# Kernel optimization log

Hardware: AMD Instinct MI355X
Metric: run time of the kernel (lower is better)

Reference implementation:

```python
import jax, jax.numpy as jnp
import numpy as np

N, E = 10000, 320000
D_IN, H1, REP, PRED_HID = 512, 512, 256, 512
TOPK = 4
EPS = 1e-5


def l2norm(x):
    return x / jnp.sqrt(jnp.sum(x * x, axis=-1, keepdims=True) + 1e-12)


def gcn_conv(x, row, col, W, b):
    # PyG GCNConv: add self loops, symmetric normalization, aggregate at col
    n = x.shape[0]
    ar = jnp.arange(n)
    r = jnp.concatenate([row, ar])
    c = jnp.concatenate([col, ar])
    w = jnp.ones(r.shape[0], x.dtype)
    deg = jax.ops.segment_sum(w, c, num_segments=n)
    dis = jnp.where(deg > 0, jax.lax.rsqrt(jnp.maximum(deg, 1e-12)), 0.0)
    norm = dis[r] * dis[c]  # [E+N]
    h = x @ W               # [N, out]
    out = jax.ops.segment_sum(norm[:, None] * h[r], c, num_segments=n)
    return out + b


def batchnorm(x, g, b):
    m = jnp.mean(x, axis=0)
    v = jnp.var(x, axis=0)
    return (x - m) * jax.lax.rsqrt(v + EPS) * g + b


def prelu(x, a):
    return jnp.where(x > 0, x, a * x)


def encoder(x, row, col, params):
    for (W, b, g, bt, a) in params:
        x = prelu(batchnorm(gcn_conv(x, row, col, W, b), g, bt), a)
    return x


def predictor(x, pW1, pb1, pg, pbb, pa, pW2, pb2):
    h = x @ pW1 + pb1
    h = prelu(batchnorm(h, pg, pbb), pa)
    return h @ pW2 + pb2


def setup_inputs():
    key = jax.random.key(0)
    ks = jax.random.split(key, 8)
    def rnd(k, shape, s=0.05):
        return jax.random.normal(k, shape, jnp.float32) * s
    return dict(
        x=jax.random.normal(ks[0], (N, D_IN), jnp.float32),
        edge_index=jax.random.randint(ks[1], (2, E), 0, N),
        neighbor_index=jax.random.randint(ks[2], (2, E), 0, N),
        W1=rnd(ks[3], (D_IN, H1)), b1=jnp.zeros((H1,), jnp.float32),
        bn1_g=jnp.ones((H1,), jnp.float32), bn1_b=jnp.zeros((H1,), jnp.float32),
        pr1=jnp.full((1,), 0.25, jnp.float32),
        W2=rnd(ks[4], (H1, REP)), b2=jnp.zeros((REP,), jnp.float32),
        bn2_g=jnp.ones((REP,), jnp.float32), bn2_b=jnp.zeros((REP,), jnp.float32),
        pr2=jnp.full((1,), 0.25, jnp.float32),
        pW1=rnd(ks[5], (REP, PRED_HID)), pb1=jnp.zeros((PRED_HID,), jnp.float32),
        pbn_g=jnp.ones((PRED_HID,), jnp.float32), pbn_b=jnp.zeros((PRED_HID,), jnp.float32),
        ppr=jnp.full((1,), 0.25, jnp.float32),
        pW2=rnd(ks[6], (PRED_HID, REP)), pb2=jnp.zeros((REP,), jnp.float32),
    )


def reference(x, edge_index, neighbor_index, W1, b1, bn1_g, bn1_b, pr1,
              W2, b2, bn2_g, bn2_b, pr2,
              pW1, pb1, pbn_g, pbn_b, ppr, pW2, pb2):
    n = x.shape[0]
    row, col = edge_index[0], edge_index[1]
    params = [(W1, b1, bn1_g, bn1_b, pr1), (W2, b2, bn2_g, bn2_b, pr2)]
    student = encoder(x, row, col, params)
    # teacher = deepcopy of student encoder at init (same params), no grad
    teacher = jax.lax.stop_gradient(encoder(x, row, col, params))
    pred = predictor(student, pW1, pb1, pbn_g, pbn_b, ppr, pW2, pb2)

    # augment_adj: per-edge similarity of normalized embeddings, densify, topk
    sn, tn = l2norm(student), l2norm(teacher)
    nrow, ncol = neighbor_index[0], neighbor_index[1]
    sim_e = jnp.sum(sn[nrow] * tn[ncol], axis=-1)                 # [E]
    S = jnp.zeros((n, n), jnp.float32).at[nrow, ncol].add(sim_e)  # coalesce sums dups
    A = jnp.zeros((n, n), jnp.bool_).at[nrow, ncol].set(True)
    _, I_knn = jax.lax.top_k(S, TOPK - 1)                          # [N, TOPK-1]

    # id loss over positive-pair levels (BGRL/AFGRL-style cosine loss)
    pn, tgt = l2norm(pred), l2norm(teacher)
    ar = jnp.arange(n)
    terms = [jnp.mean(2.0 - 2.0 * jnp.sum(pn * tgt, axis=-1))]     # self pairs
    for i in range(TOPK - 1):
        nb = I_knn[:, i]
        mask = A[ar, nb].astype(jnp.float32)  # locality = knn * adj
        c = jnp.sum(pn * tgt[nb], axis=-1)
        terms.append(jnp.sum(mask * (2.0 - 2.0 * c)) / jnp.maximum(jnp.sum(mask), 1.0))
    loss = sum(terms) / len(terms)
    return student, loss
```

## Files before the change

kernel.cpp:

```cpp
#include <hip/hip_runtime.h>
#include <math.h>

#define NN 10000
#define NE 320000
#define NXE (NE / 8)
#define SPAD 20
#define BSTR (8 * SPAD)
#define PAD 96

typedef __attribute__((ext_vector_type(8))) short bf16x8;
typedef __attribute__((ext_vector_type(4))) float f32x4;

__device__ inline unsigned short f2bf(float f) {
  unsigned u = __float_as_uint(f);
  unsigned r = (u + 0x7fffu + ((u >> 16) & 1u)) >> 16;
  return (unsigned short)r;
}
__device__ inline float bflo(unsigned u) { return __uint_as_float(u << 16); }
__device__ inline float bfhi(unsigned u) { return __uint_as_float(u & 0xffff0000u); }

#define X4 (NN * 512 / 4)
#define W1N (512 * 512)
#define W2N (512 * 256)
#define P1N (256 * 512)
#define P2N (512 * 256)
#define S1 X4
#define S2 (S1 + W1N)
#define S3 (S2 + W2N)
#define S4 (S3 + P1N)
#define PREP_TOT (S4 + P2N)

__global__ void prep_kernel(const float* __restrict__ x, unsigned short* __restrict__ xb,
    const float* __restrict__ W1, unsigned short* __restrict__ W1t,
    const float* __restrict__ W2, unsigned short* __restrict__ W2t,
    const float* __restrict__ pW1, unsigned short* __restrict__ pW1t,
    const float* __restrict__ pW2, unsigned short* __restrict__ pW2t) {
  for (int i = blockIdx.x * blockDim.x + threadIdx.x; i < PREP_TOT;
       i += gridDim.x * blockDim.x) {
    if (i < X4) {
      const float4 v = reinterpret_cast<const float4*>(x)[i];
      ushort4 o;
      o.x = f2bf(v.x); o.y = f2bf(v.y); o.z = f2bf(v.z); o.w = f2bf(v.w);
      reinterpret_cast<ushort4*>(xb)[i] = o;
    } else if (i < S2) {
      const int j = i - S1, n = j >> 9, k = j & 511;
      W1t[j] = f2bf(W1[(size_t)k * 512 + n]);
    } else if (i < S3) {
      const int j = i - S2, n = j >> 9, k = j & 511;
      W2t[j] = f2bf(W2[(size_t)k * 256 + n]);
    } else if (i < S4) {
      const int j = i - S3, n = j >> 8, k = j & 255;
      pW1t[j] = f2bf(pW1[(size_t)k * 512 + n]);
    } else {
      const int j = i - S4, n = j >> 9, k = j & 511;
      pW2t[j] = f2bf(pW2[(size_t)k * 256 + n]);
    }
  }
}

#define GBM 128
#define GBN 64
#define GBK 32
#define SAS 40

template <bool BF16OUT>
__global__ __launch_bounds__(256) void gemm_bf16(
    const unsigned short* __restrict__ A, const unsigned short* __restrict__ Bt,
    const float* __restrict__ bias, const float* __restrict__ rowscale,
    float* __restrict__ Cf, unsigned short* __restrict__ Cb,
    int M, int N, int K) {
  __shared__ unsigned short As[GBM * SAS];
  __shared__ unsigned short Bs[GBN * SAS];
  const int bm = blockIdx.y * GBM;
  const int bn = blockIdx.x * GBN;
  const int tid = threadIdx.x;
  const int wave = tid >> 6, lane = tid & 63;
  const int wm = wave & 1, wn = wave >> 1;
  f32x4 acc[4][2] = {};

  const int srow = tid >> 2;
  const int scol = (tid & 3) << 3;

  for (int k0 = 0; k0 < K; k0 += GBK) {
#pragma unroll
    for (int r = 0; r < 2; ++r) {
      const int row = srow + (r << 6);
      const int gr = bm + row;
      uint4 v = make_uint4(0u, 0u, 0u, 0u);
      if (gr < M) v = *reinterpret_cast<const uint4*>(&A[(size_t)gr * K + k0 + scol]);
      *reinterpret_cast<uint4*>(&As[row * SAS + scol]) = v;
    }
    {
      const uint4 v = *reinterpret_cast<const uint4*>(
          &Bt[(size_t)(bn + srow) * K + k0 + scol]);
      *reinterpret_cast<uint4*>(&Bs[srow * SAS + scol]) = v;
    }
    __syncthreads();
    const int kofs = (lane >> 4) << 3;
    const int rl = lane & 15;
    bf16x8 af[4], bfr[2];
#pragma unroll
    for (int m = 0; m < 4; ++m)
      af[m] = *reinterpret_cast<const bf16x8*>(
          &As[((wm << 6) + (m << 4) + rl) * SAS + kofs]);
#pragma unroll
    for (int n = 0; n < 2; ++n)
      bfr[n] = *reinterpret_cast<const bf16x8*>(
          &Bs[((wn << 5) + (n << 4) + rl) * SAS + kofs]);
#pragma unroll
    for (int m = 0; m < 4; ++m)
#pragma unroll
      for (int n = 0; n < 2; ++n)
        acc[m][n] = __builtin_amdgcn_mfma_f32_16x16x32_bf16(af[m], bfr[n], acc[m][n], 0, 0, 0);
    __syncthreads();
  }
  const int crow0 = (lane >> 4) << 2;
  const int ccol = lane & 15;
#pragma unroll
  for (int n = 0; n < 2; ++n) {
    const int col = bn + (wn << 5) + (n << 4) + ccol;
    const float bv = (!BF16OUT && bias) ? bias[col] : 0.f;
#pragma unroll
    for (int m = 0; m < 4; ++m) {
#pragma unroll
      for (int r = 0; r < 4; ++r) {
        const int rowg = bm + (wm << 6) + (m << 4) + crow0 + r;
        if (rowg < M) {
          if (BF16OUT)
            Cb[(size_t)rowg * N + col] = f2bf(acc[m][n][r] * rowscale[rowg]);
          else
            Cf[(size_t)rowg * N + col] = acc[m][n][r] + bv;
        }
      }
    }
  }
}

__global__ __launch_bounds__(256) void fill_pad8(
    const int* __restrict__ col, const int* __restrict__ row,
    int* __restrict__ cur1, unsigned short* __restrict__ ridx,
    const int* __restrict__ nrow, const int* __restrict__ ncol,
    int* __restrict__ cur2, unsigned short* __restrict__ ncidx) {
  const int x = blockIdx.x & 7;
  const int p = blockIdx.x >> 3;
  const int o = p * 256 + threadIdx.x;
  if (o >= NXE) return;
  const int e = x * NXE + o;
  {
    const int k = col[e];
    const int s = atomicAdd(&cur1[x * NN + k], 1);
    if (s < SPAD) ridx[(size_t)k * BSTR + x * SPAD + s] = (unsigned short)row[e];
  }
  {
    const int k = nrow[e];
    const int s = atomicAdd(&cur2[x * NN + k], 1);
    if (s < SPAD) ncidx[(size_t)k * BSTR + x * SPAD + s] = (unsigned short)ncol[e];
  }
}

__global__ __launch_bounds__(128) void compact_dis(
    const int* __restrict__ cur1, const unsigned short* __restrict__ rin,
    int* __restrict__ deg1, float* __restrict__ dis, unsigned short* __restrict__ rout,
    const int* __restrict__ cur2, const unsigned short* __restrict__ nin,
    int* __restrict__ deg2, unsigned short* __restrict__ nout) {
  const int j = blockIdx.x * 2 + (threadIdx.x >> 6);
  const int lane = threadIdx.x & 63;
  {
    int pre[9]; pre[0] = 0; int raw = 0;
#pragma unroll
    for (int x = 0; x < 8; ++x) {
      const int c = cur1[x * NN + j];
      raw += c;
      pre[x + 1] = pre[x] + min(c, SPAD);
    }
    const int degc = min(pre[8], PAD);
    if (lane == 0) {
      deg1[j] = degc;
      dis[j] = 1.0f / sqrtf((float)(raw + 1));
    }
    for (int t = lane; t < degc; t += 64) {
      int x = 0;
      while (t >= pre[x + 1]) ++x;
      rout[(size_t)j * PAD + t] = rin[(size_t)j * BSTR + x * SPAD + (t - pre[x])];
    }
  }
  {
    int pre[9]; pre[0] = 0;
#pragma unroll
    for (int x = 0; x < 8; ++x)
      pre[x + 1] = pre[x] + min(cur2[x * NN + j], SPAD);
    const int degc = min(pre[8], PAD);
    if (lane == 0) deg2[j] = degc;
    for (int t = lane; t < degc; t += 64) {
      int x = 0;
      while (t >= pre[x + 1]) ++x;
      nout[(size_t)j * PAD + t] = nin[(size_t)j * BSTR + x * SPAD + (t - pre[x])];
    }
  }
}

template <int C>
__global__ __launch_bounds__(128) void gcn_slice(const unsigned short* __restrict__ hs,
    const float* __restrict__ dis, const int* __restrict__ deg,
    const unsigned short* __restrict__ ridx, const float* __restrict__ bias,
    float* __restrict__ out) {
  constexpr int NS = C / 128;
  const int b = blockIdx.x;
  const int x = b & 7;
  const int p = b >> 3;
  const int slice = x & (NS - 1);
  const int pair = p * (8 / NS) + (x / NS);
  const int wave = threadIdx.x >> 6;
  const int lane = threadIdx.x & 63;
  const int j = pair * 2 + wave;
  const int g = lane >> 4;
  const int l = lane & 15;
  const int cbase = slice * 128 + l * 8;
  const unsigned short* hb = hs + cbase;

  float a[8];
  if (g == 0) {
    const uint4 v = *reinterpret_cast<const uint4*>(hb + (size_t)j * C);
    a[0] = bflo(v.x); a[1] = bfhi(v.x); a[2] = bflo(v.y); a[3] = bfhi(v.y);
    a[4] = bflo(v.z); a[5] = bfhi(v.z); a[6] = bflo(v.w); a[7] = bfhi(v.w);
  } else {
#pragma unroll
    for (int c = 0; c < 8; ++c) a[c] = 0.f;
  }
  const int e0 = j * PAD;
  const int e1 = e0 + min(deg[j], PAD);
  int e = e0 + g;
  for (; e + 4 < e1; e += 8) {
    const int r0 = ridx[e], r1 = ridx[e + 4];
    const uint4 v0 = *reinterpret_cast<const uint4*>(hb + (size_t)r0 * C);
    const uint4 v1 = *reinterpret_cast<const uint4*>(hb + (size_t)r1 * C);
    a[0] += bflo(v0.x) + bflo(v1.x); a[1] += bfhi(v0.x) + bfhi(v1.x);
    a[2] += bflo(v0.y) + bflo(v1.y); a[3] += bfhi(v0.y) + bfhi(v1.y);
    a[4] += bflo(v0.z) + bflo(v1.z); a[5] += bfhi(v0.z) + bfhi(v1.z);
    a[6] += bflo(v0.w) + bflo(v1.w); a[7] += bfhi(v0.w) + bfhi(v1.w);
  }
  if (e < e1) {
    const uint4 v = *reinterpret_cast<const uint4*>(hb + (size_t)ridx[e] * C);
    a[0] += bflo(v.x); a[1] += bfhi(v.x); a[2] += bflo(v.y); a[3] += bfhi(v.y);
    a[4] += bflo(v.z); a[5] += bfhi(v.z); a[6] += bflo(v.w); a[7] += bfhi(v.w);
  }
#pragma unroll
  for (int c = 0; c < 8; ++c) {
    a[c] += __shfl_xor(a[c], 16);
    a[c] += __shfl_xor(a[c], 32);
  }
  if (g == 0) {
    const float dj = dis[j];
    const float* bs = bias + cbase;
    float4 w0, w1;
    w0.x = fmaf(dj, a[0], bs[0]); w0.y = fmaf(dj, a[1], bs[1]);
    w0.z = fmaf(dj, a[2], bs[2]); w0.w = fmaf(dj, a[3], bs[3]);
    w1.x = fmaf(dj, a[4], bs[4]); w1.y = fmaf(dj, a[5], bs[5]);
    w1.z = fmaf(dj, a[6], bs[6]); w1.w = fmaf(dj, a[7], bs[7]);
    float* o = out + (size_t)j * C + cbase;
    *reinterpret_cast<float4*>(o) = w0;
    *reinterpret_cast<float4*>(o + 4) = w1;
  }
}

template <int C>
__global__ __launch_bounds__(256) void bn_stats(const float* __restrict__ x,
    float* __restrict__ sums, float* __restrict__ sqs, int n) {
  constexpr int P = C / 256;
  float s[P], q[P];
#pragma unroll
  for (int p = 0; p < P; ++p) { s[p] = 0.f; q[p] = 0.f; }
  const int rpb = (n + gridDim.x - 1) / gridDim.x;
  const int r0 = blockIdx.x * rpb;
  const int r1 = min(r0 + rpb, n);
  for (int r = r0; r < r1; ++r) {
#pragma unroll
    for (int p = 0; p < P; ++p) {
      const float v = x[(size_t)r * C + threadIdx.x + (p << 8)];
      s[p] += v;
      q[p] = fmaf(v, v, q[p]);
    }
  }
#pragma unroll
  for (int p = 0; p < P; ++p) {
    atomicAdd(&sums[threadIdx.x + (p << 8)], s[p]);
    atomicAdd(&sqs[threadIdx.x + (p << 8)], q[p]);
  }
}

__device__ inline void bn_coeff(const float* sums, const float* sqs,
                                const float* g, const float* b, int c,
                                float inv_n, float& sc, float& sh) {
  const float m = sums[c] * inv_n;
  const float var = sqs[c] * inv_n - m * m;
  sc = g[c] / sqrtf(var + 1e-5f);
  sh = b[c] - m * sc;
}

__global__ void bn_apply_prelu(const float* __restrict__ in,
    unsigned short* __restrict__ outb, const float* __restrict__ sums,
    const float* __restrict__ sqs, const float* __restrict__ g,
    const float* __restrict__ b, const float* __restrict__ pa,
    float inv_n, int total4, int cmask) {
  const float a = pa[0];
  for (int i = blockIdx.x * blockDim.x + threadIdx.x; i < total4;
       i += gridDim.x * blockDim.x) {
    float4 v = reinterpret_cast<const float4*>(in)[i];
    const int c0 = (i << 2) & cmask;
    float r[4] = {v.x, v.y, v.z, v.w};
    ushort4 o;
    unsigned short* op = reinterpret_cast<unsigned short*>(&o);
#pragma unroll
    for (int j = 0; j < 4; ++j) {
      float sc, sh;
      bn_coeff(sums, sqs, g, b, c0 + j, inv_n, sc, sh);
      float t = fmaf(r[j], sc, sh);
      t = t > 0.f ? t : a * t;
      op[j] = f2bf(t);
    }
    reinterpret_cast<ushort4*>(outb)[i] = o;
  }
}

__global__ __launch_bounds__(128) void bn_l2_student(float* __restrict__ student,
    unsigned short* __restrict__ stb, unsigned short* __restrict__ snb,
    const float* __restrict__ sums, const float* __restrict__ sqs,
    const float* __restrict__ g, const float* __restrict__ b,
    const float* __restrict__ pa, float inv_n) {
  const int r = blockIdx.x * 2 + (threadIdx.x >> 6);
  const int t = threadIdx.x & 63;
  const float a = pa[0];
  const float4 v = reinterpret_cast<const float4*>(student + (size_t)r * 256)[t];
  float w[4] = {v.x, v.y, v.z, v.w};
  const int c0 = t << 2;
#pragma unroll
  for (int j = 0; j < 4; ++j) {
    float sc, sh;
    bn_coeff(sums, sqs, g, b, c0 + j, inv_n, sc, sh);
    float u = fmaf(w[j], sc, sh);
    w[j] = u > 0.f ? u : a * u;
  }
  reinterpret_cast<float4*>(student + (size_t)r * 256)[t] =
      make_float4(w[0], w[1], w[2], w[3]);
  ushort4 ob;
  ob.x = f2bf(w[0]); ob.y = f2bf(w[1]); ob.z = f2bf(w[2]); ob.w = f2bf(w[3]);
  reinterpret_cast<ushort4*>(stb + (size_t)r * 256)[t] = ob;
  float sq = w[0] * w[0] + w[1] * w[1] + w[2] * w[2] + w[3] * w[3];
#pragma unroll
  for (int o = 1; o < 64; o <<= 1) sq += __shfl_xor(sq, o);
  const float inv = 1.0f / sqrtf(sq + 1e-12f);
  ushort4 on;
  on.x = f2bf(w[0] * inv); on.y = f2bf(w[1] * inv);
  on.z = f2bf(w[2] * inv); on.w = f2bf(w[3] * inv);
  reinterpret_cast<ushort4*>(snb + (size_t)r * 256)[t] = on;
}

__global__ __launch_bounds__(128) void topk_kernel(const unsigned short* __restrict__ snb,
    const int* __restrict__ deg, const unsigned short* __restrict__ ncidx,
    int* __restrict__ nb) {
  const int wv = threadIdx.x >> 6, lane = threadIdx.x & 63;
  const int i = blockIdx.x * 2 + wv;
  __shared__ unsigned short sni[2][256];
  __shared__ float vals[2][PAD];
  __shared__ int   cols[2][PAD];
  __shared__ float mvals[2][PAD];
  __shared__ int   mcols[2][PAD];
  reinterpret_cast<uint2*>(sni[wv])[lane] =
      reinterpret_cast<const uint2*>(snb + (size_t)i * 256)[lane];
  __syncthreads();
  const int e0 = i * PAD;
  const int k  = deg[i];
  for (int e = lane; e < k; e += 64) {
    const int j = ncidx[e0 + e];
    const uint4* bj = reinterpret_cast<const uint4*>(snb + (size_t)j * 256);
    const uint4* aj = reinterpret_cast<const uint4*>(sni[wv]);
    float s = 0.f;
#pragma unroll 8
    for (int q = 0; q < 32; ++q) {
      const uint4 b = bj[q];
      const uint4 a = aj[q];
      s = fmaf(bflo(a.x), bflo(b.x), s);
      s = fmaf(bfhi(a.x), bfhi(b.x), s);
      s = fmaf(bflo(a.y), bflo(b.y), s);
      s = fmaf(bfhi(a.y), bfhi(b.y), s);
      s = fmaf(bflo(a.z), bflo(b.z), s);
      s = fmaf(bfhi(a.z), bfhi(b.z), s);
      s = fmaf(bflo(a.w), bflo(b.w), s);
      s = fmaf(bfhi(a.w), bfhi(b.w), s);
    }
    vals[wv][e] = s;
    cols[wv][e] = j;
  }
  __syncthreads();
  for (int e = lane; e < k; e += 64) {
    const int c = cols[wv][e];
    bool first = true;
    float sum = vals[wv][e];
    for (int q = 0; q < k; ++q) {
      if (q == e) continue;
      if (cols[wv][q] == c) {
        if (q < e) { first = false; break; }
        sum += vals[wv][q];
      }
    }
    mvals[wv][e] = sum;
    mcols[wv][e] = first ? c : -1;
  }
  __syncthreads();
  for (int s = 0; s < 3; ++s) {
    unsigned long long best = 0ull;
    for (int e = lane; e < k; e += 64) {
      const int c = mcols[wv][e];
      if (c < 0) continue;
      const float v = mvals[wv][e];
      if (v <= 0.f) continue;
      const unsigned long long key =
          ((unsigned long long)__float_as_uint(v) << 32) |
          (unsigned long long)(0xFFFFFFFFu - (unsigned)c);
      if (key > best) best = key;
    }
#pragma unroll
    for (int off = 1; off < 64; off <<= 1) {
      const unsigned long long o = __shfl_xor(best, off);
      if (o > best) best = o;
    }
    const int wcol = best ? (int)(0xFFFFFFFFu - (unsigned)(best & 0xFFFFFFFFu)) : -1;
    if (lane == 0) nb[i * 3 + s] = wcol;
    if (wcol >= 0)
      for (int e = lane; e < k; e += 64)
        if (mcols[wv][e] == wcol) mcols[wv][e] = -1;
    __syncthreads();
  }
}

__global__ __launch_bounds__(256) void loss_terms(const float* __restrict__ pred,
    const unsigned short* __restrict__ snb, const int* __restrict__ nb,
    float* __restrict__ part, int n) {
  const int t = threadIdx.x, wave = t >> 6, lane = t & 63;
  const int r = blockIdx.x * 4 + wave;
  float vals[7] = {0.f, 0.f, 0.f, 0.f, 0.f, 0.f, 0.f};
  if (r < n) {
    const float4 p = reinterpret_cast<const float4*>(pred + (size_t)r * 256)[lane];
    float sq = p.x * p.x + p.y * p.y + p.z * p.z + p.w * p.w;
#pragma unroll
    for (int o = 1; o < 64; o <<= 1) sq += __shfl_xor(sq, o);
    const float inv = 1.0f / sqrtf(sq + 1e-12f);
    const float a0 = p.x * inv, a1 = p.y * inv, a2 = p.z * inv, a3 = p.w * inv;
    {
      const uint2 bv = reinterpret_cast<const uint2*>(snb + (size_t)r * 256)[lane];
      float d = a0 * bflo(bv.x) + a1 * bfhi(bv.x) + a2 * bflo(bv.y) + a3 * bfhi(bv.y);
#pragma unroll
      for (int o = 1; o < 64; o <<= 1) d += __shfl_xor(d, o);
      vals[0] = 2.f - 2.f * d;
    }
    for (int s = 0; s < 3; ++s) {
      const int j = nb[r * 3 + s];
      if (j >= 0) {
        const uint2 cv = reinterpret_cast<const uint2*>(snb + (size_t)j * 256)[lane];
        float e = a0 * bflo(cv.x) + a1 * bfhi(cv.x) + a2 * bflo(cv.y) + a3 * bfhi(cv.y);
#pragma unroll
        for (int o = 1; o < 64; o <<= 1) e += __shfl_xor(e, o);
        vals[1 + s] = 2.f - 2.f * e;
        vals[4 + s] = 1.f;
      }
    }
  }
  __shared__ float red[4][7];
  if (lane == 0)
    for (int q = 0; q < 7; ++q) red[wave][q] = vals[q];
  __syncthreads();
  if (t < 7)
    part[(size_t)blockIdx.x * 8 + t] =
        red[0][t] + red[1][t] + red[2][t] + red[3][t];
}

__global__ __launch_bounds__(64) void finalize_loss(const float* __restrict__ part,
    float* __restrict__ out, int nblocks, int n) {
  const int lane = threadIdx.x;
  float comp[7] = {0.f, 0.f, 0.f, 0.f, 0.f, 0.f, 0.f};
  for (int b = lane; b < nblocks; b += 64) {
#pragma unroll
    for (int q = 0; q < 7; ++q) comp[q] += part[(size_t)b * 8 + q];
  }
#pragma unroll
  for (int q = 0; q < 7; ++q) {
#pragma unroll
    for (int o = 1; o < 64; o <<= 1) comp[q] += __shfl_xor(comp[q], o);
  }
  if (lane == 0) {
    float loss = comp[0] / n;
    for (int s = 0; s < 3; ++s) loss += comp[1 + s] / fmaxf(comp[4 + s], 1.f);
    out[0] = loss * 0.25f;
  }
}

extern "C" void kernel_launch(void* const* d_in, const int* in_sizes, int n_in,
                              void* d_out, int out_size, void* d_ws, size_t ws_size,
                              hipStream_t stream) {
  const float* x   = (const float*)d_in[0];
  const int*   eidx = (const int*)d_in[1];
  const int*   nidx = (const int*)d_in[2];
  const float* W1  = (const float*)d_in[3];
  const float* b1  = (const float*)d_in[4];
  const float* g1  = (const float*)d_in[5];
  const float* bb1 = (const float*)d_in[6];
  const float* pr1 = (const float*)d_in[7];
  const float* W2  = (const float*)d_in[8];
  const float* b2  = (const float*)d_in[9];
  const float* g2  = (const float*)d_in[10];
  const float* bb2 = (const float*)d_in[11];
  const float* pr2 = (const float*)d_in[12];
  const float* pW1 = (const float*)d_in[13];
  const float* pb1 = (const float*)d_in[14];
  const float* pg  = (const float*)d_in[15];
  const float* pbb = (const float*)d_in[16];
  const float* ppr = (const float*)d_in[17];
  const float* pW2 = (const float*)d_in[18];
  const float* pb2 = (const float*)d_in[19];

  const int* row  = eidx;
  const int* col  = eidx + NE;
  const int* nrow = nidx;
  const int* ncol = nidx + NE;

  float* student = (float*)d_out;
  float* loss    = student + (size_t)NN * 256;

  char* ws = (char*)d_ws;
  size_t off = 0;
  auto take = [&](size_t bytes) -> void* {
    void* p = ws + off;
    off += (bytes + 255) & ~(size_t)255;
    return p;
  };
  const int LOSS_NB = NN / 4;
  const size_t zstart = off;
  int*   cur1 = (int*)take((size_t)8 * NN * 4);
  int*   cur2 = (int*)take((size_t)8 * NN * 4);
  float* bns1 = (float*)take(1024 * 4);
  float* bns2 = (float*)take(512 * 4);
  float* bns3 = (float*)take(1024 * 4);
  const size_t zsize = off - zstart;
  float* h1    = (float*)take((size_t)NN * 512 * 4);
  float* x2    = (float*)take((size_t)NN * 512 * 4);
  float* h2    = (float*)take((size_t)NN * 256 * 4);
  float* dis   = (float*)take((size_t)NN * 4);
  int*   deg1  = (int*)take((size_t)NN * 4);
  int*   deg2  = (int*)take((size_t)NN * 4);
  unsigned short* ridxr  = (unsigned short*)take((size_t)NN * BSTR * 2);
  unsigned short* ncidxr = (unsigned short*)take((size_t)NN * BSTR * 2);
  unsigned short* ridx   = (unsigned short*)take((size_t)NN * PAD * 2);
  unsigned short* ncidx  = (unsigned short*)take((size_t)NN * PAD * 2);
  int*   nb    = (int*)take((size_t)NN * 3 * 4);
  float* part  = (float*)take((size_t)LOSS_NB * 8 * 4);
  unsigned short* xb   = (unsigned short*)take((size_t)NN * 512 * 2);
  unsigned short* x2b  = (unsigned short*)take((size_t)NN * 512 * 2);
  unsigned short* stb  = (unsigned short*)take((size_t)NN * 256 * 2);
  unsigned short* phb  = (unsigned short*)take((size_t)NN * 512 * 2);
  unsigned short* h1b  = (unsigned short*)take((size_t)NN * 512 * 2);
  unsigned short* h2b  = (unsigned short*)take((size_t)NN * 256 * 2);
  unsigned short* snb  = (unsigned short*)take((size_t)NN * 256 * 2);
  unsigned short* W1t  = (unsigned short*)take((size_t)W1N * 2);
  unsigned short* W2t  = (unsigned short*)take((size_t)W2N * 2);
  unsigned short* pW1t = (unsigned short*)take((size_t)P1N * 2);
  unsigned short* pW2t = (unsigned short*)take((size_t)P2N * 2);

  float* ph   = h1;
  float* pred = h2;

  const int MB = (NN + GBM - 1) / GBM;
  const float inv_n = 1.0f / (float)NN;

  prep_kernel<<<2048, 256, 0, stream>>>(x, xb, W1, W1t, W2, W2t, pW1, pW1t, pW2, pW2t);
  hipMemsetAsync((char*)d_ws + zstart, 0, zsize, stream);

  fill_pad8<<<1280, 256, 0, stream>>>(col, row, cur1, ridxr, nrow, ncol, cur2, ncidxr);
  compact_dis<<<NN / 2, 128, 0, stream>>>(cur1, ridxr, deg1, dis, ridx,
                                          cur2, ncidxr, deg2, ncidx);

  { dim3 g(512 / GBN, MB);
    gemm_bf16<true><<<g, 256, 0, stream>>>(xb, W1t, nullptr, dis, nullptr, h1b,
                                           NN, 512, 512); }
  gcn_slice<512><<<NN * 4 / 2, 128, 0, stream>>>(h1b, dis, deg1, ridx, b1, x2);
  bn_stats<512><<<256, 256, 0, stream>>>(x2, bns1, bns1 + 512, NN);
  bn_apply_prelu<<<2048, 256, 0, stream>>>(x2, x2b, bns1, bns1 + 512, g1, bb1, pr1,
                                           inv_n, NN * 512 / 4, 511);

  { dim3 g(256 / GBN, MB);
    gemm_bf16<true><<<g, 256, 0, stream>>>(x2b, W2t, nullptr, dis, nullptr, h2b,
                                           NN, 256, 512); }
  gcn_slice<256><<<NN * 2 / 2, 128, 0, stream>>>(h2b, dis, deg1, ridx, b2, student);
  bn_stats<256><<<256, 256, 0, stream>>>(student, bns2, bns2 + 256, NN);
  bn_l2_student<<<NN / 2, 128, 0, stream>>>(student, stb, snb, bns2, bns2 + 256,
                                            g2, bb2, pr2, inv_n);

  topk_kernel<<<NN / 2, 128, 0, stream>>>(snb, deg2, ncidx, nb);

  { dim3 g(512 / GBN, MB);
    gemm_bf16<false><<<g, 256, 0, stream>>>(stb, pW1t, pb1, nullptr, ph, nullptr,
                                            NN, 512, 256); }
  bn_stats<512><<<256, 256, 0, stream>>>(ph, bns3, bns3 + 512, NN);
  bn_apply_prelu<<<2048, 256, 0, stream>>>(ph, phb, bns3, bns3 + 512, pg, pbb, ppr,
                                           inv_n, NN * 512 / 4, 511);
  { dim3 g(256 / GBN, MB);
    gemm_bf16<false><<<g, 256, 0, stream>>>(phb, pW2t, pb2, nullptr, pred, nullptr,
                                            NN, 256, 512); }

  loss_terms<<<LOSS_NB, 256, 0, stream>>>(pred, snb, nb, part, NN);
  finalize_loss<<<1, 64, 0, stream>>>(part, loss, LOSS_NB, NN);
}
```

Before: 309.9 us.

## Store 512-wide intermediates in bf16, tile weight transposes, fold memset into prep

The layer-1 GCN output and the predictor hidden activations are now written in bf16 instead of fp32. BatchNorm statistics are read from those bf16 buffers and applied in place, which roughly halves the traffic for these large intermediates. The weight transpose moves to a shared-memory tiled kernel so reads and writes are coalesced, and the workspace memset is folded into the prep kernel. In exchange, BN statistics are computed on rounded bf16 values, which slightly changes numerics.

```diff
diff --git a/kernel.cpp b/kernel.cpp
--- a/kernel.cpp
+++ b/kernel.cpp
@@ -24,37 +24,49 @@
 #define W2N (512 * 256)
 #define P1N (256 * 512)
 #define P2N (512 * 256)
-#define S1 X4
-#define S2 (S1 + W1N)
-#define S3 (S2 + W2N)
-#define S4 (S3 + P1N)
-#define PREP_TOT (S4 + P2N)
 
 __global__ void prep_kernel(const float* __restrict__ x, unsigned short* __restrict__ xb,
-    const float* __restrict__ W1, unsigned short* __restrict__ W1t,
-    const float* __restrict__ W2, unsigned short* __restrict__ W2t,
-    const float* __restrict__ pW1, unsigned short* __restrict__ pW1t,
-    const float* __restrict__ pW2, unsigned short* __restrict__ pW2t) {
-  for (int i = blockIdx.x * blockDim.x + threadIdx.x; i < PREP_TOT;
+                            uint4* __restrict__ zbase, int zn) {
+  const int tot = X4 + zn;
+  for (int i = blockIdx.x * blockDim.x + threadIdx.x; i < tot;
        i += gridDim.x * blockDim.x) {
     if (i < X4) {
       const float4 v = reinterpret_cast<const float4*>(x)[i];
       ushort4 o;
       o.x = f2bf(v.x); o.y = f2bf(v.y); o.z = f2bf(v.z); o.w = f2bf(v.w);
       reinterpret_cast<ushort4*>(xb)[i] = o;
-    } else if (i < S2) {
-      const int j = i - S1, n = j >> 9, k = j & 511;
-      W1t[j] = f2bf(W1[(size_t)k * 512 + n]);
-    } else if (i < S3) {
-      const int j = i - S2, n = j >> 9, k = j & 511;
-      W2t[j] = f2bf(W2[(size_t)k * 256 + n]);
-    } else if (i < S4) {
-      const int j = i - S3, n = j >> 8, k = j & 255;
-      pW1t[j] = f2bf(pW1[(size_t)k * 512 + n]);
     } else {
-      const int j = i - S4, n = j >> 9, k = j & 511;
-      pW2t[j] = f2bf(pW2[(size_t)k * 256 + n]);
-    }
+      zbase[i - X4] = make_uint4(0u, 0u, 0u, 0u);
+    }
+  }
+}
+
+__global__ __launch_bounds__(256) void wtrans(
+    const float* __restrict__ W1, unsigned short* __restrict__ W1t,
+    const float* __restrict__ W2, unsigned short* __restrict__ W2t,
+    const float* __restrict__ pW1, unsigned short* __restrict__ pW1t,
+    const float* __restrict__ pW2, unsigned short* __restrict__ pW2t) {
+  __shared__ float tile[32][33];
+  int b = blockIdx.x;
+  const float* W; unsigned short* Wt; int K, N, tn_tiles;
+  if (b < 256)      { W = W1;  Wt = W1t;  K = 512; N = 512; tn_tiles = 16; }
+  else if (b < 384) { W = W2;  Wt = W2t;  K = 512; N = 256; tn_tiles = 8;  b -= 256; }
+  else if (b < 512) { W = pW1; Wt = pW1t; K = 256; N = 512; tn_tiles = 16; b -= 384; }
+  else              { W = pW2; Wt = pW2t; K = 512; N = 256; tn_tiles = 8;  b -= 512; }
+  const int tk = b / tn_tiles, tn = b - tk * tn_tiles;
+  const int t = threadIdx.x;
+  const int nn = t & 31, kq = t >> 5;
+#pragma unroll
+  for (int p = 0; p < 4; ++p) {
+    const int kk = kq + p * 8;
+    tile[kk][nn] = W[(size_t)(tk * 32 + kk) * N + tn * 32 + nn];
+  }
+  __syncthreads();
+  const int kk2 = t & 31, nq = t >> 5;
+#pragma unroll
+  for (int p = 0; p < 4; ++p) {
+    const int n = nq + p * 8;
+    Wt[(size_t)(tn * 32 + n) * K + tk * 32 + kk2] = f2bf(tile[kk2][n]);
   }
 }
 
@@ -63,7 +75,7 @@
 #define GBK 32
 #define SAS 40
 
-template <bool BF16OUT>
+template <int MODE>
 __global__ __launch_bounds__(256) void gemm_bf16(
     const unsigned short* __restrict__ A, const unsigned short* __restrict__ Bt,
     const float* __restrict__ bias, const float* __restrict__ rowscale,
@@ -119,15 +131,17 @@
 #pragma unroll
   for (int n = 0; n < 2; ++n) {
     const int col = bn + (wn << 5) + (n << 4) + ccol;
-    const float bv = (!BF16OUT && bias) ? bias[col] : 0.f;
+    const float bv = (MODE != 1 && bias) ? bias[col] : 0.f;
 #pragma unroll
     for (int m = 0; m < 4; ++m) {
 #pragma unroll
       for (int r = 0; r < 4; ++r) {
         const int rowg = bm + (wm << 6) + (m << 4) + crow0 + r;
         if (rowg < M) {
-          if (BF16OUT)
+          if (MODE == 1)
             Cb[(size_t)rowg * N + col] = f2bf(acc[m][n][r] * rowscale[rowg]);
+          else if (MODE == 2)
+            Cb[(size_t)rowg * N + col] = f2bf(acc[m][n][r] + bv);
           else
             Cf[(size_t)rowg * N + col] = acc[m][n][r] + bv;
         }
@@ -199,11 +213,11 @@
   }
 }
 
-template <int C>
+template <int C, bool BF16OUT>
 __global__ __launch_bounds__(128) void gcn_slice(const unsigned short* __restrict__ hs,
     const float* __restrict__ dis, const int* __restrict__ deg,
     const unsigned short* __restrict__ ridx, const float* __restrict__ bias,
-    float* __restrict__ out) {
+    float* __restrict__ outf, unsigned short* __restrict__ outb) {
   constexpr int NS = C / 128;
   const int b = blockIdx.x;
   const int x = b & 7;
@@ -252,15 +266,45 @@
   if (g == 0) {
     const float dj = dis[j];
     const float* bs = bias + cbase;
-    float4 w0, w1;
-    w0.x = fmaf(dj, a[0], bs[0]); w0.y = fmaf(dj, a[1], bs[1]);
-    w0.z = fmaf(dj, a[2], bs[2]); w0.w = fmaf(dj, a[3], bs[3]);
-    w1.x = fmaf(dj, a[4], bs[4]); w1.y = fmaf(dj, a[5], bs[5]);
-    w1.z = fmaf(dj, a[6], bs[6]); w1.w = fmaf(dj, a[7], bs[7]);
-    float* o = out + (size_t)j * C + cbase;
-    *reinterpret_cast<float4*>(o) = w0;
-    *reinterpret_cast<float4*>(o + 4) = w1;
-  }
+    float w[8];
+#pragma unroll
+    for (int c = 0; c < 8; ++c) w[c] = fmaf(dj, a[c], bs[c]);
+    if (BF16OUT) {
+      ushort4 o0, o1;
+      o0.x = f2bf(w[0]); o0.y = f2bf(w[1]); o0.z = f2bf(w[2]); o0.w = f2bf(w[3]);
+      o1.x = f2bf(w[4]); o1.y = f2bf(w[5]); o1.z = f2bf(w[6]); o1.w = f2bf(w[7]);
+      unsigned short* o = outb + (size_t)j * C + cbase;
+      *reinterpret_cast<ushort4*>(o) = o0;
+      *reinterpret_cast<ushort4*>(o + 4) = o1;
+    } else {
+      float* o = outf + (size_t)j * C + cbase;
+      *reinterpret_cast<float4*>(o) = make_float4(w[0], w[1], w[2], w[3]);
+      *reinterpret_cast<float4*>(o + 4) = make_float4(w[4], w[5], w[6], w[7]);
+    }
+  }
+}
+
+template <int C>
+__global__ __launch_bounds__(256) void bn_stats_b(const unsigned short* __restrict__ x,
+    float* __restrict__ sums, float* __restrict__ sqs, int n) {
+  constexpr int P = C / 512;
+  static_assert(C == 512, "bn_stats_b assumes C=512");
+  float s0 = 0.f, s1 = 0.f, q0 = 0.f, q1 = 0.f;
+  const int t = threadIdx.x;
+  const int rpb = (n + gridDim.x - 1) / gridDim.x;
+  const int r0 = blockIdx.x * rpb;
+  const int r1 = min(r0 + rpb, n);
+  for (int r = r0; r < r1; ++r) {
+    const unsigned v = reinterpret_cast<const unsigned*>(x + (size_t)r * C)[t];
+    const float a = bflo(v), b = bfhi(v);
+    s0 += a; q0 = fmaf(a, a, q0);
+    s1 += b; q1 = fmaf(b, b, q1);
+  }
+  atomicAdd(&sums[2 * t + 0], s0);
+  atomicAdd(&sums[2 * t + 1], s1);
+  atomicAdd(&sqs[2 * t + 0], q0);
+  atomicAdd(&sqs[2 * t + 1], q1);
+  (void)P;
 }
 
 template <int C>
@@ -297,17 +341,16 @@
   sh = b[c] - m * sc;
 }
 
-__global__ void bn_apply_prelu(const float* __restrict__ in,
-    unsigned short* __restrict__ outb, const float* __restrict__ sums,
-    const float* __restrict__ sqs, const float* __restrict__ g,
-    const float* __restrict__ b, const float* __restrict__ pa,
-    float inv_n, int total4, int cmask) {
+__global__ void bn_apply_b(unsigned short* __restrict__ xb,
+    const float* __restrict__ sums, const float* __restrict__ sqs,
+    const float* __restrict__ g, const float* __restrict__ b,
+    const float* __restrict__ pa, float inv_n, int total4, int cmask) {
   const float a = pa[0];
   for (int i = blockIdx.x * blockDim.x + threadIdx.x; i < total4;
        i += gridDim.x * blockDim.x) {
-    float4 v = reinterpret_cast<const float4*>(in)[i];
+    uint2 v = reinterpret_cast<const uint2*>(xb)[i];
     const int c0 = (i << 2) & cmask;
-    float r[4] = {v.x, v.y, v.z, v.w};
+    float r[4] = {bflo(v.x), bfhi(v.x), bflo(v.y), bfhi(v.y)};
     ushort4 o;
     unsigned short* op = reinterpret_cast<unsigned short*>(&o);
 #pragma unroll
@@ -318,7 +361,7 @@
       t = t > 0.f ? t : a * t;
       op[j] = f2bf(t);
     }
-    reinterpret_cast<ushort4*>(outb)[i] = o;
+    reinterpret_cast<ushort4*>(xb)[i] = o;
   }
 }
 
@@ -541,8 +584,6 @@
   float* bns2 = (float*)take(512 * 4);
   float* bns3 = (float*)take(1024 * 4);
   const size_t zsize = off - zstart;
-  float* h1    = (float*)take((size_t)NN * 512 * 4);
-  float* x2    = (float*)take((size_t)NN * 512 * 4);
   float* h2    = (float*)take((size_t)NN * 256 * 4);
   float* dis   = (float*)take((size_t)NN * 4);
   int*   deg1  = (int*)take((size_t)NN * 4);
@@ -565,31 +606,33 @@
   unsigned short* pW1t = (unsigned short*)take((size_t)P1N * 2);
   unsigned short* pW2t = (unsigned short*)take((size_t)P2N * 2);
 
-  float* ph   = h1;
   float* pred = h2;
 
   const int MB = (NN + GBM - 1) / GBM;
   const float inv_n = 1.0f / (float)NN;
 
-  prep_kernel<<<2048, 256, 0, stream>>>(x, xb, W1, W1t, W2, W2t, pW1, pW1t, pW2, pW2t);
-  hipMemsetAsync((char*)d_ws + zstart, 0, zsize, stream);
+  prep_kernel<<<2048, 256, 0, stream>>>(x, xb, (uint4*)((char*)d_ws + zstart),
+                                        (int)(zsize / 16));
+  wtrans<<<640, 256, 0, stream>>>(W1, W1t, W2, W2t, pW1, pW1t, pW2, pW2t);
 
   fill_pad8<<<1280, 256, 0, stream>>>(col, row, cur1, ridxr, nrow, ncol, cur2, ncidxr);
   compact_dis<<<NN / 2, 128, 0, stream>>>(cur1, ridxr, deg1, dis, ridx,
                                           cur2, ncidxr, deg2, ncidx);
 
   { dim3 g(512 / GBN, MB);
-    gemm_bf16<true><<<g, 256, 0, stream>>>(xb, W1t, nullptr, dis, nullptr, h1b,
-                                           NN, 512, 512); }
-  gcn_slice<512><<<NN * 4 / 2, 128, 0, stream>>>(h1b, dis, deg1, ridx, b1, x2);
-  bn_stats<512><<<256, 256, 0, stream>>>(x2, bns1, bns1 + 512, NN);
-  bn_apply_prelu<<<2048, 256, 0, stream>>>(x2, x2b, bns1, bns1 + 512, g1, bb1, pr1,
-                                           inv_n, NN * 512 / 4, 511);
+    gemm_bf16<1><<<g, 256, 0, stream>>>(xb, W1t, nullptr, dis, nullptr, h1b,
+                                        NN, 512, 512); }
+  gcn_slice<512, true><<<NN * 4 / 2, 128, 0, stream>>>(h1b, dis, deg1, ridx, b1,
+                                                       nullptr, x2b);
+  bn_stats_b<512><<<256, 256, 0, stream>>>(x2b, bns1, bns1 + 512, NN);
+  bn_apply_b<<<2048, 256, 0, stream>>>(x2b, bns1, bns1 + 512, g1, bb1, pr1,
+                                       inv_n, NN * 512 / 4, 511);
 
   { dim3 g(256 / GBN, MB);
-    gemm_bf16<true><<<g, 256, 0, stream>>>(x2b, W2t, nullptr, dis, nullptr, h2b,
-                                           NN, 256, 512); }
-  gcn_slice<256><<<NN * 2 / 2, 128, 0, stream>>>(h2b, dis, deg1, ridx, b2, student);
+    gemm_bf16<1><<<g, 256, 0, stream>>>(x2b, W2t, nullptr, dis, nullptr, h2b,
+                                        NN, 256, 512); }
+  gcn_slice<256, false><<<NN * 2 / 2, 128, 0, stream>>>(h2b, dis, deg1, ridx, b2,
+                                                        student, nullptr);
   bn_stats<256><<<256, 256, 0, stream>>>(student, bns2, bns2 + 256, NN);
   bn_l2_student<<<NN / 2, 128, 0, stream>>>(student, stb, snb, bns2, bns2 + 256,
                                             g2, bb2, pr2, inv_n);
@@ -597,14 +640,14 @@
   topk_kernel<<<NN / 2, 128, 0, stream>>>(snb, deg2, ncidx, nb);
 
   { dim3 g(512 / GBN, MB);
-    gemm_bf16<false><<<g, 256, 0, stream>>>(stb, pW1t, pb1, nullptr, ph, nullptr,
-                                            NN, 512, 256); }
-  bn_stats<512><<<256, 256, 0, stream>>>(ph, bns3, bns3 + 512, NN);
-  bn_apply_prelu<<<2048, 256, 0, stream>>>(ph, phb, bns3, bns3 + 512, pg, pbb, ppr,
-                                           inv_n, NN * 512 / 4, 511);
+    gemm_bf16<2><<<g, 256, 0, stream>>>(stb, pW1t, pb1, nullptr, nullptr, phb,
+                                        NN, 512, 256); }
+  bn_stats_b<512><<<256, 256, 0, stream>>>(phb, bns3, bns3 + 512, NN);
+  bn_apply_b<<<2048, 256, 0, stream>>>(phb, bns3, bns3 + 512, pg, pbb, ppr,
+                                       inv_n, NN * 512 / 4, 511);
   { dim3 g(256 / GBN, MB);
-    gemm_bf16<false><<<g, 256, 0, stream>>>(phb, pW2t, pb2, nullptr, pred, nullptr,
-                                            NN, 256, 512); }
+    gemm_bf16<0><<<g, 256, 0, stream>>>(phb, pW2t, pb2, nullptr, pred, nullptr,
+                                        NN, 256, 512); }
 
   loss_terms<<<LOSS_NB, 256, 0, stream>>>(pred, snb, nb, part, NN);
   finalize_loss<<<1, 64, 0, stream>>>(part, loss, LOSS_NB, NN);
```

New measurement: 323.0 us. 4.2% more time.
